# Kernel optimization log

Hardware: AMD Instinct MI355X
Metric: run time of the kernel (lower is better)

Reference implementation:

```python
import jax, jax.numpy as jnp
import numpy as np

HEADS = 4
KD = 32          # key_dim per head
LEVELS = 2
G = 3            # 2**dims - 1 HP orientation groups
STRENGTH = 0.25
DECAY = 0.6
LN_EPS = 1e-5
MIX_EPS = 1e-3


def _layernorm(x, g, b):
    m = jnp.mean(x, axis=-1, keepdims=True)
    v = jnp.var(x, axis=-1, keepdims=True)
    return (x - m) * jax.lax.rsqrt(v + LN_EPS) * g + b


def _dwt2(x):
    # Haar analysis, periodic/even sizes. [B,H,W,C] -> [B,H/2,W/2,4C] (LL,LH,HL,HH)
    x00 = x[:, 0::2, 0::2]; x01 = x[:, 0::2, 1::2]
    x10 = x[:, 1::2, 0::2]; x11 = x[:, 1::2, 1::2]
    ll = (x00 + x01 + x10 + x11) * 0.5
    lh = (x00 - x01 + x10 - x11) * 0.5
    hl = (x00 + x01 - x10 - x11) * 0.5
    hh = (x00 - x01 - x10 + x11) * 0.5
    return jnp.concatenate([ll, lh, hl, hh], axis=-1)


def _idwt2(w):
    # exact Haar synthesis: [B,H/2,W/2,4C] -> [B,H,W,C]
    ll, lh, hl, hh = jnp.split(w, 4, axis=-1)
    x00 = (ll + lh + hl + hh) * 0.5
    x01 = (ll - lh + hl - hh) * 0.5
    x10 = (ll + lh - hl - hh) * 0.5
    x11 = (ll - lh - hl + hh) * 0.5
    B, H2, W2, C = ll.shape
    r0 = jnp.stack([x00, x01], axis=3).reshape(B, H2, 2 * W2, C)  # interleave W
    r1 = jnp.stack([x10, x11], axis=3).reshape(B, H2, 2 * W2, C)
    return jnp.stack([r0, r1], axis=2).reshape(B, 2 * H2, 2 * W2, C)  # interleave H


def _axial_mhsa(x, p):
    # AxialMHSAND: sequential sweep over spatial axes; each pass is
    # proj(attn(softmax(QK^T/sqrt(d)) V)) on norm(x), qkv via 1x1 conv (=matmul).
    g, b, wq, bq, wk, bk, wv, bv, wp, bp = p
    scale = KD ** -0.5
    for axis in (1, 2):
        X = _layernorm(x, g, b)
        B, H, W, _ = X.shape
        Q = (X @ wq + bq).reshape(B, H, W, HEADS, KD)
        K = (X @ wk + bk).reshape(B, H, W, HEADS, KD)
        V = (X @ wv + bv).reshape(B, H, W, HEADS, KD)
        if axis == 1:  # attend along H, batch over (B, W, heads)
            A = jax.nn.softmax(jnp.einsum('bqwnd,bkwnd->bwnqk', Q, K) * scale, axis=-1)
            Y = jnp.einsum('bwnqk,bkwnd->bqwnd', A, V)
        else:          # attend along W, batch over (B, H, heads)
            A = jax.nn.softmax(jnp.einsum('bhqnd,bhknd->bhnqk', Q, K) * scale, axis=-1)
            Y = jnp.einsum('bhnqk,bhknd->bhqnd', A, V)
        x = Y.reshape(B, H, W, HEADS * KD) @ wp + bp
    return x


def setup_inputs() -> dict:
    key = jax.random.key(0)
    ks = jax.random.split(key, 24)
    C = 64
    HD = HEADS * KD
    s = 0.02
    inp = {'x': jax.random.normal(ks[0], (4, 256, 256, C), jnp.float32)}
    i = 1
    for pre in ('lp', 'hp'):
        inp[pre + '_ln_g'] = jnp.ones((C,), jnp.float32)
        inp[pre + '_ln_b'] = jnp.zeros((C,), jnp.float32)
        inp[pre + '_wq'] = jax.random.normal(ks[i], (C, HD), jnp.float32) * s
        inp[pre + '_bq'] = jax.random.normal(ks[i + 1], (HD,), jnp.float32) * s
        inp[pre + '_wk'] = jax.random.normal(ks[i + 2], (C, HD), jnp.float32) * s
        inp[pre + '_bk'] = jax.random.normal(ks[i + 3], (HD,), jnp.float32) * s
        inp[pre + '_wv'] = jax.random.normal(ks[i + 4], (C, HD), jnp.float32) * s
        inp[pre + '_bv'] = jax.random.normal(ks[i + 5], (HD,), jnp.float32) * s
        inp[pre + '_wp'] = jax.random.normal(ks[i + 6], (HD, C), jnp.float32) * s
        inp[pre + '_bp'] = jax.random.normal(ks[i + 7], (C,), jnp.float32) * s
        i += 8
    mix = jnp.eye(G, dtype=jnp.float32) + MIX_EPS * (jnp.ones((G, G), jnp.float32) - jnp.eye(G, dtype=jnp.float32))
    inp['mix_w0'] = mix
    inp['mix_w1'] = mix
    return inp


def reference(x, lp_ln_g, lp_ln_b, lp_wq, lp_bq, lp_wk, lp_bk, lp_wv, lp_bv, lp_wp, lp_bp,
              hp_ln_g, hp_ln_b, hp_wq, hp_bq, hp_wk, hp_bk, hp_wv, hp_bv, hp_wp, hp_bp,
              mix_w0, mix_w1):
    lp_p = (lp_ln_g, lp_ln_b, lp_wq, lp_bq, lp_wk, lp_bk, lp_wv, lp_bv, lp_wp, lp_bp)
    hp_p = (hp_ln_g, hp_ln_b, hp_wq, hp_bq, hp_wk, hp_bk, hp_wv, hp_bv, hp_wp, hp_bp)
    mix_ws = [mix_w0, mix_w1]
    C = x.shape[-1]
    cur = x
    hps = []
    for _ in range(LEVELS):  # analysis pyramid
        w = _dwt2(cur)
        hps.append(w[..., C:])
        cur = w[..., :C]
    # deepest LP: axial attention, residual with full strength
    cur = cur + STRENGTH * _axial_mhsa(cur, lp_p)
    for l in reversed(range(LEVELS)):  # synthesis with per-level HP processing
        hp = hps[l]
        B, H2, W2, _ = hp.shape
        gain = STRENGTH * (DECAY ** (LEVELS - 1 - l))  # coarser levels stronger
        hp_g = hp.reshape(B, H2, W2, G, C)
        mixed = jnp.einsum('gd,bhwdc->bhwgc', mix_ws[l], hp_g)  # OrientationMix
        batched = mixed.transpose(3, 0, 1, 2, 4).reshape(G * B, H2, W2, C)
        att = _axial_mhsa(batched, hp_p)  # shared hp_attn across groups/levels
        att = att.reshape(G, B, H2, W2, C).transpose(1, 2, 3, 0, 4).reshape(B, H2, W2, G * C)
        hp_out = hp + gain * att
        cur = _idwt2(jnp.concatenate([cur, hp_out], axis=-1))
    return cur
```

## Files before the change

### kernel.cpp

```cpp
#include <hip/hip_runtime.h>

#define LN_EPS 1e-5f

typedef __attribute__((ext_vector_type(8))) short bf16x8;
typedef __attribute__((ext_vector_type(4))) float f32x4;

#define MFMA16(A, B, C) __builtin_amdgcn_mfma_f32_16x16x32_bf16(A, B, C, 0, 0, 0)

static __device__ __forceinline__ unsigned short f2bf_rne(float f) {
    union { unsigned int i; float f; } c; c.f = f;
    unsigned int i = c.i;
    return (unsigned short)((i + 0x7fffu + ((i >> 16) & 1u)) >> 16);
}
static __device__ __forceinline__ void bfstore2(unsigned short* p, float x, float y) {
    *(unsigned int*)p = (unsigned int)f2bf_rne(x) | ((unsigned int)f2bf_rne(y) << 16);
}
static __device__ __forceinline__ unsigned pk2(float a, float b) {
    return __builtin_amdgcn_perm(__builtin_bit_cast(unsigned, b),
                                 __builtin_bit_cast(unsigned, a), 0x07060302u);
}
static __device__ __forceinline__ unsigned short tb16(float f) {
    return (unsigned short)(__builtin_bit_cast(unsigned, f) >> 16);
}

__global__ void dwt_kernel(const float4* __restrict__ in, float4* __restrict__ ll,
                           float4* __restrict__ hp, int B, int H2, int W2) {
    const int i = blockIdx.x * blockDim.x + threadIdx.x;
    const int total = B * H2 * W2 * 16;
    if (i >= total) return;
    const int c4 = i & 15;
    int t = i >> 4;
    const int w2 = t % W2; t /= W2;
    const int h2 = t % H2;
    const int b = t / H2;
    const int W = W2 * 2;
    const size_t base = (((size_t)b * (H2 * 2) + 2 * h2) * W + 2 * w2) * 16 + c4;
    const float4 x00 = in[base];
    const float4 x01 = in[base + 16];
    const float4 x10 = in[base + (size_t)W * 16];
    const float4 x11 = in[base + (size_t)W * 16 + 16];
    float4 vll, vlh, vhl, vhh;
#define DWTC(a) \
    vll.a = (x00.a + x01.a + x10.a + x11.a) * 0.5f; \
    vlh.a = (x00.a - x01.a + x10.a - x11.a) * 0.5f; \
    vhl.a = (x00.a + x01.a - x10.a - x11.a) * 0.5f; \
    vhh.a = (x00.a - x01.a - x10.a + x11.a) * 0.5f;
    DWTC(x) DWTC(y) DWTC(z) DWTC(w)
#undef DWTC
    const size_t oi = ((size_t)b * H2 + h2) * W2 + w2;
    ll[oi * 16 + c4] = vll;
    hp[oi * 48 + c4] = vlh;
    hp[oi * 48 + 16 + c4] = vhl;
    hp[oi * 48 + 32 + c4] = vhh;
}

__global__ void idwt_kernel(const float4* __restrict__ cur, const float4* __restrict__ hp,
                            const float4* __restrict__ att, float gain,
                            float4* __restrict__ out, int B, int H2, int W2) {
    const int i = blockIdx.x * blockDim.x + threadIdx.x;
    const int total = B * H2 * W2 * 16;
    if (i >= total) return;
    const int c4 = i & 15;
    int t = i >> 4;
    const int w2 = t % W2; t /= W2;
    const int h2 = t % H2;
    const int b = t / H2;
    const size_t oi = ((size_t)b * H2 + h2) * W2 + w2;
    const size_t sp = (size_t)h2 * W2 + w2;
    const size_t gstr = (size_t)B * H2 * W2;
    const float4 vll = cur[oi * 16 + c4];
    float4 vlh = hp[oi * 48 + c4];
    float4 vhl = hp[oi * 48 + 16 + c4];
    float4 vhh = hp[oi * 48 + 32 + c4];
    const float4 a0 = att[((size_t)b * H2 * W2 + sp) * 16 + c4];
    const float4 a1 = att[((size_t)b * H2 * W2 + gstr + sp) * 16 + c4];
    const float4 a2 = att[((size_t)b * H2 * W2 + 2 * gstr + sp) * 16 + c4];
#define ADDG(a) \
    vlh.a = fmaf(gain, a0.a, vlh.a); \
    vhl.a = fmaf(gain, a1.a, vhl.a); \
    vhh.a = fmaf(gain, a2.a, vhh.a);
    ADDG(x) ADDG(y) ADDG(z) ADDG(w)
#undef ADDG
    float4 x00, x01, x10, x11;
#define IDWTC(a) \
    x00.a = (vll.a + vlh.a + vhl.a + vhh.a) * 0.5f; \
    x01.a = (vll.a - vlh.a + vhl.a - vhh.a) * 0.5f; \
    x10.a = (vll.a + vlh.a - vhl.a - vhh.a) * 0.5f; \
    x11.a = (vll.a - vlh.a - vhl.a + vhh.a) * 0.5f;
    IDWTC(x) IDWTC(y) IDWTC(z) IDWTC(w)
#undef IDWTC
    const int W = W2 * 2;
    const size_t r0 = (((size_t)b * (H2 * 2) + 2 * h2) * W + 2 * w2) * 16 + c4;
    out[r0] = x00;
    out[r0 + 16] = x01;
    out[r0 + (size_t)W * 16] = x10;
    out[r0 + (size_t)W * 16 + 16] = x11;
}

__global__ void mix_kernel(const float4* __restrict__ hp, const float* __restrict__ mixw,
                           float4* __restrict__ outb, int B, int HW) {
    const int i = blockIdx.x * blockDim.x + threadIdx.x;
    const int total = 3 * B * HW * 16;
    if (i >= total) return;
    const int c4 = i & 15;
    int t = i >> 4;
    const int p = t % HW; t /= HW;
    const int b = t % B;
    const int g = t / B;
    const float m0 = mixw[g * 3 + 0];
    const float m1 = mixw[g * 3 + 1];
    const float m2 = mixw[g * 3 + 2];
    const size_t hb = ((size_t)b * HW + p) * 48 + c4;
    const float4 h0 = hp[hb];
    const float4 h1 = hp[hb + 16];
    const float4 h2 = hp[hb + 32];
    float4 r;
    r.x = m0 * h0.x + m1 * h1.x + m2 * h2.x;
    r.y = m0 * h0.y + m1 * h1.y + m2 * h2.y;
    r.z = m0 * h0.z + m1 * h1.z + m2 * h2.z;
    r.w = m0 * h0.w + m1 * h1.w + m2 * h2.w;
    outb[i] = r;
}

__global__ void prep_weights(const float* __restrict__ lwq, const float* __restrict__ lwk,
                             const float* __restrict__ lwv, const float* __restrict__ lwp,
                             const float* __restrict__ hwq, const float* __restrict__ hwk,
                             const float* __restrict__ hwv, const float* __restrict__ hwp,
                             unsigned short* __restrict__ wbuf) {
    const int i = blockIdx.x * blockDim.x + threadIdx.x;
    if (i >= 65536) return;
    const int set = i >> 15;
    const int r = i & 32767;
    const float* wq = set ? hwq : lwq;
    const float* wk = set ? hwk : lwk;
    const float* wv = set ? hwv : lwv;
    const float* wp = set ? hwp : lwp;
    float v;
    if (r < 24576) {
        const int nn = r >> 6, c = r & 63;
        const float* w = (nn < 128) ? wq : (nn < 256) ? wk : wv;
        v = w[c * 128 + (nn & 127)];
    } else {
        const int r2 = r - 24576;
        const int nn = r2 >> 7, d = r2 & 127;
        v = wp[d * 64 + nn];
    }
    wbuf[i] = f2bf_rne(v);
}

template<int S>
__global__ __launch_bounds__(S * 4)
void axial_attn(const float* __restrict__ xin, float* __restrict__ xout,
                const float* __restrict__ basep, float res_scale, int axis,
                const float* __restrict__ ln_g, const float* __restrict__ ln_b,
                const float* __restrict__ bq, const float* __restrict__ bk,
                const float* __restrict__ bv, const float* __restrict__ bp,
                const unsigned short* __restrict__ wqkvT,
                const unsigned short* __restrict__ wpT)
{
    constexpr int BS = S * 4;
    constexpr int NW = BS / 64;
    constexpr int XSTR = 72;
    constexpr int QSTR = 136;
    constexpr int PSTR = S + 8;
    constexpr int NTPW = 24 / NW;

    __shared__ __align__(16) unsigned short Xs[S * XSTR];
    __shared__ __align__(16) unsigned short Qs[S * QSTR];
    __shared__ __align__(16) unsigned short Ks[S * QSTR];
    __shared__ __align__(16) unsigned short Vt[128 * PSTR];
    __shared__ __align__(16) unsigned short Pb[NW * 16 * PSTR];

    const int tid = threadIdx.x;
    const int lane = tid & 63;
    const int w = tid >> 6;
    const int n16 = lane & 15;
    const int quad = lane >> 4;

    const int line = blockIdx.x;
    const int lb = line / S;
    const int lr = line - lb * S;
    size_t lbase, tstr;
    if (axis == 1) { lbase = ((size_t)lb * S * S + lr) * 64; tstr = (size_t)S * 64; }
    else           { lbase = ((size_t)lb * S + lr) * (size_t)S * 64; tstr = 64; }

    {
        const float4* x4 = (const float4*)xin;
        const size_t lbase4 = lbase >> 2, tstr4 = tstr >> 2;
        const int sub = tid & 15;
        const float4 g4 = ((const float4*)ln_g)[sub];
        const float4 be4 = ((const float4*)ln_b)[sub];
        for (int t = (tid >> 4); t < S; t += BS / 16) {
            float4 v = x4[lbase4 + (size_t)t * tstr4 + sub];
            float s = v.x + v.y + v.z + v.w;
            float ss = v.x * v.x + v.y * v.y + v.z * v.z + v.w * v.w;
            #pragma unroll
            for (int m = 1; m < 16; m <<= 1) {
                s += __shfl_xor(s, m);
                ss += __shfl_xor(ss, m);
            }
            const float mean = s * 0.015625f;
            const float rstd = rsqrtf(ss * 0.015625f - mean * mean + LN_EPS);
            unsigned short* xr = &Xs[t * XSTR + sub * 4];
            bfstore2(xr,     (v.x - mean) * rstd * g4.x + be4.x,
                             (v.y - mean) * rstd * g4.y + be4.y);
            bfstore2(xr + 2, (v.z - mean) * rstd * g4.z + be4.z,
                             (v.w - mean) * rstd * g4.w + be4.w);
        }
    }
    __syncthreads();

    {
        for (int i = 0; i < NTPW; ++i) {
            const int nt = w * NTPW + i;
            const int region = nt >> 3;
            const int cbase = (nt & 7) * 16;
            const float* bias_base = (region == 0) ? bq : (region == 1) ? bk : bv;
            const float bias = bias_base[cbase + n16];
            const bf16x8 B0 = *(const bf16x8*)&wqkvT[(nt * 16 + n16) * 64 + quad * 8];
            const bf16x8 B1 = *(const bf16x8*)&wqkvT[(nt * 16 + n16) * 64 + 32 + quad * 8];
            for (int mt = 0; mt < S / 16; ++mt) {
                const bf16x8 A0 = *(const bf16x8*)&Xs[(mt * 16 + n16) * XSTR + quad * 8];
                const bf16x8 A1 = *(const bf16x8*)&Xs[(mt * 16 + n16) * XSTR + 32 + quad * 8];
                f32x4 acc = {bias, bias, bias, bias};
                acc = MFMA16(A0, B0, acc);
                acc = MFMA16(A1, B1, acc);
                if (region < 2) {
                    unsigned short* dst = (region == 0) ? Qs : Ks;
                    const int row0 = mt * 16 + quad * 4;
                    #pragma unroll
                    for (int r = 0; r < 4; ++r)
                        dst[(row0 + r) * QSTR + cbase + n16] = tb16(acc[r]);
                } else {
                    const int d = cbase + n16;
                    const unsigned p01 = pk2(acc[0], acc[1]);
                    const unsigned p23 = pk2(acc[2], acc[3]);
                    *(uint2*)&Vt[d * PSTR + mt * 16 + quad * 4] = make_uint2(p01, p23);
                }
            }
        }
    }
    __syncthreads();

    {
        constexpr int WPH = NW / 4;
        const int h = w / WPH;
        const int sub = w - h * WPH;
        const int hoff = h * 32;
        unsigned short* pbw = &Pb[w * 16 * PSTR];
        const float qs = 0.17677669529663687f * 1.4426950408889634f;
        const bf16x8 ones = (bf16x8)(short)0x3F80;

        bf16x8 vb[2][S / 32];
        #pragma unroll
        for (int nt2 = 0; nt2 < 2; ++nt2)
            #pragma unroll
            for (int kt = 0; kt < S / 32; ++kt)
                vb[nt2][kt] = *(const bf16x8*)&Vt[(hoff + nt2 * 16 + n16) * PSTR + kt * 32 + quad * 8];

        for (int si = 0; si < 4; ++si) {
            const int q0 = (sub * 4 + si) * 16;
            const bf16x8 qb = *(const bf16x8*)&Qs[(q0 + n16) * QSTR + hoff + quad * 8];
            for (int mt = 0; mt < S / 16; ++mt) {
                const bf16x8 ka = *(const bf16x8*)&Ks[(mt * 16 + n16) * QSTR + hoff + quad * 8];
                f32x4 sc = {0.f, 0.f, 0.f, 0.f};
                sc = MFMA16(ka, qb, sc);
                const float e0 = __builtin_amdgcn_exp2f(sc[0] * qs);
                const float e1 = __builtin_amdgcn_exp2f(sc[1] * qs);
                const float e2 = __builtin_amdgcn_exp2f(sc[2] * qs);
                const float e3 = __builtin_amdgcn_exp2f(sc[3] * qs);
                *(uint2*)&pbw[n16 * PSTR + mt * 16 + quad * 4] =
                    make_uint2(pk2(e0, e1), pk2(e2, e3));
            }
            f32x4 accl = {0.f, 0.f, 0.f, 0.f};
            f32x4 y0 = {0.f, 0.f, 0.f, 0.f};
            f32x4 y1 = {0.f, 0.f, 0.f, 0.f};
            for (int kt = 0; kt < S / 32; ++kt) {
                const bf16x8 pa = *(const bf16x8*)&pbw[n16 * PSTR + kt * 32 + quad * 8];
                accl = MFMA16(pa, ones, accl);
                y0 = MFMA16(pa, vb[0][kt], y0);
                y1 = MFMA16(pa, vb[1][kt], y1);
            }
            #pragma unroll
            for (int r = 0; r < 4; ++r) {
                const float inv = __builtin_amdgcn_rcpf(accl[r]);
                const int row = q0 + quad * 4 + r;
                Qs[row * QSTR + hoff + n16]      = tb16(y0[r] * inv);
                Qs[row * QSTR + hoff + 16 + n16] = tb16(y1[r] * inv);
            }
        }
    }
    __syncthreads();

    {
        const int m0 = w * 16;
        bf16x8 pa[4];
        #pragma unroll
        for (int kt = 0; kt < 4; ++kt)
            pa[kt] = *(const bf16x8*)&Qs[(m0 + n16) * QSTR + kt * 32 + quad * 8];
        #pragma unroll
        for (int nt = 0; nt < 4; ++nt) {
            const float bias = bp[nt * 16 + n16];
            f32x4 acc = {bias, bias, bias, bias};
            #pragma unroll
            for (int kt = 0; kt < 4; ++kt) {
                const bf16x8 wb = *(const bf16x8*)&wpT[(nt * 16 + n16) * 128 + kt * 32 + quad * 8];
                acc = MFMA16(pa[kt], wb, acc);
            }
            #pragma unroll
            for (int r = 0; r < 4; ++r) {
                const size_t gi = lbase + (size_t)(m0 + quad * 4 + r) * tstr + nt * 16 + n16;
                float v = acc[r];
                if (basep) v = fmaf(res_scale, v, basep[gi]);
                xout[gi] = v;
            }
        }
    }
}

extern "C" void kernel_launch(void* const* d_in, const int* in_sizes, int n_in,
                              void* d_out, int out_size, void* d_ws, size_t ws_size,
                              hipStream_t stream) {
    (void)in_sizes; (void)n_in; (void)out_size; (void)ws_size;
    const float* x = (const float*)d_in[0];
    const float* P_lp[10];
    const float* P_hp[10];
    for (int i = 0; i < 10; ++i) P_lp[i] = (const float*)d_in[1 + i];
    for (int i = 0; i < 10; ++i) P_hp[i] = (const float*)d_in[11 + i];
    const float* mw0 = (const float*)d_in[21];
    const float* mw1 = (const float*)d_in[22];
    float* out = (float*)d_out;
    float* ws = (float*)d_ws;

    float* ll0 = ws;
    float* hp0 = ll0 + (size_t)4194304;
    float* t0  = hp0 + (size_t)12582912;
    float* ll1  = t0;
    float* hp1  = t0 + (size_t)1048576;
    float* ta2  = t0 + (size_t)4194304;
    float* lpta = t0 + (size_t)7340032;
    float* tb  = out;
    float* t1b = out;
    unsigned short* wbuf = (unsigned short*)(out + (size_t)13631488);

    prep_weights<<<256, 256, 0, stream>>>(
        P_lp[2], P_lp[4], P_lp[6], P_lp[8],
        P_hp[2], P_hp[4], P_hp[6], P_hp[8], wbuf);

    dwt_kernel<<<4 * 128 * 128 * 16 / 256, 256, 0, stream>>>(
        (const float4*)x, (float4*)ll0, (float4*)hp0, 4, 128, 128);
    dwt_kernel<<<4 * 64 * 64 * 16 / 256, 256, 0, stream>>>(
        (const float4*)ll0, (float4*)ll1, (float4*)hp1, 4, 64, 64);

    const unsigned short* lp_qkvT = wbuf;
    const unsigned short* lp_wpT  = wbuf + 24576;
    const unsigned short* hp_qkvT = wbuf + 32768;
    const unsigned short* hp_wpT  = wbuf + 32768 + 24576;

#define ATTN(S_, GRID_, XIN_, XOUT_, BASE_, RS_, P_, QKVT_, WPT_, AX_) \
    axial_attn<S_><<<GRID_, (S_) * 4, 0, stream>>>(XIN_, XOUT_, BASE_, RS_, AX_, \
        P_[0], P_[1], P_[3], P_[5], P_[7], P_[9], QKVT_, WPT_)

    ATTN(64, 4 * 64, ll1, lpta, (const float*)nullptr, 1.f, P_lp, lp_qkvT, lp_wpT, 1);
    ATTN(64, 4 * 64, lpta, ll1, ll1, 0.25f, P_lp, lp_qkvT, lp_wpT, 2);

    mix_kernel<<<3 * 4 * 64 * 64 * 16 / 256, 256, 0, stream>>>(
        (const float4*)hp1, mw1, (float4*)ta2, 4, 64 * 64);
    ATTN(64, 12 * 64, ta2, tb, (const float*)nullptr, 1.f, P_hp, hp_qkvT, hp_wpT, 1);
    ATTN(64, 12 * 64, tb, ta2, (const float*)nullptr, 1.f, P_hp, hp_qkvT, hp_wpT, 2);
    idwt_kernel<<<4 * 64 * 64 * 16 / 256, 256, 0, stream>>>(
        (const float4*)ll1, (const float4*)hp1, (const float4*)ta2, 0.25f,
        (float4*)ll0, 4, 64, 64);

    mix_kernel<<<3 * 4 * 128 * 128 * 16 / 256, 256, 0, stream>>>(
        (const float4*)hp0, mw0, (float4*)t0, 4, 128 * 128);
    ATTN(128, 12 * 128, t0, t1b, (const float*)nullptr, 1.f, P_hp, hp_qkvT, hp_wpT, 1);
    ATTN(128, 12 * 128, t1b, t0, (const float*)nullptr, 1.f, P_hp, hp_qkvT, hp_wpT, 2);
    idwt_kernel<<<4 * 128 * 128 * 16 / 256, 256, 0, stream>>>(
        (const float4*)ll0, (const float4*)hp0, (const float4*)t0, 0.15f,
        (float4*)out, 4, 128, 128);
#undef ATTN
}
```

Measured before the change: 486.7 us.

## Fuse orientation mix into attention, batch LP/HP passes, fold softmax scale into Wq

Removes the standalone mix kernels by computing the orientation mix inside the attention load stage. The LP and level-1 HP attention passes now run as one grouped launch using a job struct, which cuts launches and fills the GPU better. The softmax scale times log2(e) is folded into the Q weights and bias, removing a multiply before exp2. The QKV projection loop is restructured so B fragments stay in registers, K fragments are hoisted into registers, and launch bounds request 2 blocks per CU, which raises register pressure.

```diff
diff --git a/kernel.cpp b/kernel.cpp
--- a/kernel.cpp
+++ b/kernel.cpp
@@ -1,6 +1,7 @@
 #include <hip/hip_runtime.h>
 
 #define LN_EPS 1e-5f
+#define QSCALE 0.25500526578425445f
 
 typedef __attribute__((ext_vector_type(8))) short bf16x8;
 typedef __attribute__((ext_vector_type(4))) float f32x4;
@@ -97,31 +98,6 @@
     out[r0 + (size_t)W * 16 + 16] = x11;
 }
 
-__global__ void mix_kernel(const float4* __restrict__ hp, const float* __restrict__ mixw,
-                           float4* __restrict__ outb, int B, int HW) {
-    const int i = blockIdx.x * blockDim.x + threadIdx.x;
-    const int total = 3 * B * HW * 16;
-    if (i >= total) return;
-    const int c4 = i & 15;
-    int t = i >> 4;
-    const int p = t % HW; t /= HW;
-    const int b = t % B;
-    const int g = t / B;
-    const float m0 = mixw[g * 3 + 0];
-    const float m1 = mixw[g * 3 + 1];
-    const float m2 = mixw[g * 3 + 2];
-    const size_t hb = ((size_t)b * HW + p) * 48 + c4;
-    const float4 h0 = hp[hb];
-    const float4 h1 = hp[hb + 16];
-    const float4 h2 = hp[hb + 32];
-    float4 r;
-    r.x = m0 * h0.x + m1 * h1.x + m2 * h2.x;
-    r.y = m0 * h0.y + m1 * h1.y + m2 * h2.y;
-    r.z = m0 * h0.z + m1 * h1.z + m2 * h2.z;
-    r.w = m0 * h0.w + m1 * h1.w + m2 * h2.w;
-    outb[i] = r;
-}
-
 __global__ void prep_weights(const float* __restrict__ lwq, const float* __restrict__ lwk,
                              const float* __restrict__ lwv, const float* __restrict__ lwp,
                              const float* __restrict__ hwq, const float* __restrict__ hwk,
@@ -140,6 +116,7 @@
         const int nn = r >> 6, c = r & 63;
         const float* w = (nn < 128) ? wq : (nn < 256) ? wk : wv;
         v = w[c * 128 + (nn & 127)];
+        if (nn < 128) v *= QSCALE;
     } else {
         const int r2 = r - 24576;
         const int nn = r2 >> 7, d = r2 & 127;
@@ -148,15 +125,22 @@
     wbuf[i] = f2bf_rne(v);
 }
 
+struct Job {
+    const float* xin;
+    const float* mixsrc;
+    const float* mixw;
+    float* xout;
+    const float* basep;
+    float res_scale;
+    const float* ln_g; const float* ln_b;
+    const float* bq; const float* bk; const float* bv; const float* bp;
+    const unsigned short* wqkvT;
+    const unsigned short* wpT;
+};
+
 template<int S>
-__global__ __launch_bounds__(S * 4)
-void axial_attn(const float* __restrict__ xin, float* __restrict__ xout,
-                const float* __restrict__ basep, float res_scale, int axis,
-                const float* __restrict__ ln_g, const float* __restrict__ ln_b,
-                const float* __restrict__ bq, const float* __restrict__ bk,
-                const float* __restrict__ bv, const float* __restrict__ bp,
-                const unsigned short* __restrict__ wqkvT,
-                const unsigned short* __restrict__ wpT)
+__global__ __launch_bounds__(S * 4, 2)
+void axial_attn(Job jA, Job jB, int nA, int axis)
 {
     constexpr int BS = S * 4;
     constexpr int NW = BS / 64;
@@ -177,7 +161,9 @@
     const int n16 = lane & 15;
     const int quad = lane >> 4;
 
-    const int line = blockIdx.x;
+    const bool isB = (int)blockIdx.x >= nA;
+    const Job j = isB ? jB : jA;
+    const int line = isB ? (int)blockIdx.x - nA : (int)blockIdx.x;
     const int lb = line / S;
     const int lr = line - lb * S;
     size_t lbase, tstr;
@@ -185,13 +171,33 @@
     else           { lbase = ((size_t)lb * S + lr) * (size_t)S * 64; tstr = 64; }
 
     {
-        const float4* x4 = (const float4*)xin;
+        const int sub = tid & 15;
+        const float4 g4 = ((const float4*)j.ln_g)[sub];
+        const float4 be4 = ((const float4*)j.ln_b)[sub];
+        const float4* x4 = (const float4*)j.xin;
+        const float4* hp4 = (const float4*)j.mixsrc;
         const size_t lbase4 = lbase >> 2, tstr4 = tstr >> 2;
-        const int sub = tid & 15;
-        const float4 g4 = ((const float4*)ln_g)[sub];
-        const float4 be4 = ((const float4*)ln_b)[sub];
+        float m0, m1, m2; int bimg;
+        if (hp4) {
+            const int g = lb >> 2;
+            bimg = lb & 3;
+            m0 = j.mixw[g * 3 + 0]; m1 = j.mixw[g * 3 + 1]; m2 = j.mixw[g * 3 + 2];
+        }
         for (int t = (tid >> 4); t < S; t += BS / 16) {
-            float4 v = x4[lbase4 + (size_t)t * tstr4 + sub];
+            float4 v;
+            if (hp4) {
+                const int pos = (axis == 1) ? (t * S + lr) : (lr * S + t);
+                const size_t hb = ((size_t)bimg * S * S + pos) * 48 + sub;
+                const float4 h0 = hp4[hb];
+                const float4 h1 = hp4[hb + 16];
+                const float4 h2 = hp4[hb + 32];
+                v.x = m0 * h0.x + m1 * h1.x + m2 * h2.x;
+                v.y = m0 * h0.y + m1 * h1.y + m2 * h2.y;
+                v.z = m0 * h0.z + m1 * h1.z + m2 * h2.z;
+                v.w = m0 * h0.w + m1 * h1.w + m2 * h2.w;
+            } else {
+                v = x4[lbase4 + (size_t)t * tstr4 + sub];
+            }
             float s = v.x + v.y + v.z + v.w;
             float ss = v.x * v.x + v.y * v.y + v.z * v.z + v.w * v.w;
             #pragma unroll
@@ -211,20 +217,31 @@
     __syncthreads();
 
     {
+        bf16x8 Bf0[NTPW], Bf1[NTPW];
+        float biasv[NTPW];
+        #pragma unroll
         for (int i = 0; i < NTPW; ++i) {
             const int nt = w * NTPW + i;
             const int region = nt >> 3;
             const int cbase = (nt & 7) * 16;
-            const float* bias_base = (region == 0) ? bq : (region == 1) ? bk : bv;
-            const float bias = bias_base[cbase + n16];
-            const bf16x8 B0 = *(const bf16x8*)&wqkvT[(nt * 16 + n16) * 64 + quad * 8];
-            const bf16x8 B1 = *(const bf16x8*)&wqkvT[(nt * 16 + n16) * 64 + 32 + quad * 8];
-            for (int mt = 0; mt < S / 16; ++mt) {
-                const bf16x8 A0 = *(const bf16x8*)&Xs[(mt * 16 + n16) * XSTR + quad * 8];
-                const bf16x8 A1 = *(const bf16x8*)&Xs[(mt * 16 + n16) * XSTR + 32 + quad * 8];
-                f32x4 acc = {bias, bias, bias, bias};
-                acc = MFMA16(A0, B0, acc);
-                acc = MFMA16(A1, B1, acc);
+            const float* bias_base = (region == 0) ? j.bq : (region == 1) ? j.bk : j.bv;
+            float bias = bias_base[cbase + n16];
+            if (region == 0) bias *= QSCALE;
+            biasv[i] = bias;
+            Bf0[i] = *(const bf16x8*)&j.wqkvT[(nt * 16 + n16) * 64 + quad * 8];
+            Bf1[i] = *(const bf16x8*)&j.wqkvT[(nt * 16 + n16) * 64 + 32 + quad * 8];
+        }
+        for (int mt = 0; mt < S / 16; ++mt) {
+            const bf16x8 A0 = *(const bf16x8*)&Xs[(mt * 16 + n16) * XSTR + quad * 8];
+            const bf16x8 A1 = *(const bf16x8*)&Xs[(mt * 16 + n16) * XSTR + 32 + quad * 8];
+            #pragma unroll
+            for (int i = 0; i < NTPW; ++i) {
+                const int nt = w * NTPW + i;
+                const int region = nt >> 3;
+                const int cbase = (nt & 7) * 16;
+                f32x4 acc = {biasv[i], biasv[i], biasv[i], biasv[i]};
+                acc = MFMA16(A0, Bf0[i], acc);
+                acc = MFMA16(A1, Bf1[i], acc);
                 if (region < 2) {
                     unsigned short* dst = (region == 0) ? Qs : Ks;
                     const int row0 = mt * 16 + quad * 4;
@@ -233,9 +250,8 @@
                         dst[(row0 + r) * QSTR + cbase + n16] = tb16(acc[r]);
                 } else {
                     const int d = cbase + n16;
-                    const unsigned p01 = pk2(acc[0], acc[1]);
-                    const unsigned p23 = pk2(acc[2], acc[3]);
-                    *(uint2*)&Vt[d * PSTR + mt * 16 + quad * 4] = make_uint2(p01, p23);
+                    *(uint2*)&Vt[d * PSTR + mt * 16 + quad * 4] =
+                        make_uint2(pk2(acc[0], acc[1]), pk2(acc[2], acc[3]));
                 }
             }
         }
@@ -248,38 +264,43 @@
         const int sub = w - h * WPH;
         const int hoff = h * 32;
         unsigned short* pbw = &Pb[w * 16 * PSTR];
-        const float qs = 0.17677669529663687f * 1.4426950408889634f;
         const bf16x8 ones = (bf16x8)(short)0x3F80;
 
-        bf16x8 vb[2][S / 32];
-        #pragma unroll
-        for (int nt2 = 0; nt2 < 2; ++nt2)
-            #pragma unroll
-            for (int kt = 0; kt < S / 32; ++kt)
-                vb[nt2][kt] = *(const bf16x8*)&Vt[(hoff + nt2 * 16 + n16) * PSTR + kt * 32 + quad * 8];
-
+        bf16x8 vb0[S / 32], vb1[S / 32];
+        #pragma unroll
+        for (int kt = 0; kt < S / 32; ++kt) {
+            vb0[kt] = *(const bf16x8*)&Vt[(hoff + n16) * PSTR + kt * 32 + quad * 8];
+            vb1[kt] = *(const bf16x8*)&Vt[(hoff + 16 + n16) * PSTR + kt * 32 + quad * 8];
+        }
+        bf16x8 ka[S / 16];
+        #pragma unroll
+        for (int mt = 0; mt < S / 16; ++mt)
+            ka[mt] = *(const bf16x8*)&Ks[(mt * 16 + n16) * QSTR + hoff + quad * 8];
+
+        #pragma unroll
         for (int si = 0; si < 4; ++si) {
             const int q0 = (sub * 4 + si) * 16;
             const bf16x8 qb = *(const bf16x8*)&Qs[(q0 + n16) * QSTR + hoff + quad * 8];
+            #pragma unroll
             for (int mt = 0; mt < S / 16; ++mt) {
-                const bf16x8 ka = *(const bf16x8*)&Ks[(mt * 16 + n16) * QSTR + hoff + quad * 8];
                 f32x4 sc = {0.f, 0.f, 0.f, 0.f};
-                sc = MFMA16(ka, qb, sc);
-                const float e0 = __builtin_amdgcn_exp2f(sc[0] * qs);
-                const float e1 = __builtin_amdgcn_exp2f(sc[1] * qs);
-                const float e2 = __builtin_amdgcn_exp2f(sc[2] * qs);
-                const float e3 = __builtin_amdgcn_exp2f(sc[3] * qs);
+                sc = MFMA16(ka[mt], qb, sc);
+                const float e0 = __builtin_amdgcn_exp2f(sc[0]);
+                const float e1 = __builtin_amdgcn_exp2f(sc[1]);
+                const float e2 = __builtin_amdgcn_exp2f(sc[2]);
+                const float e3 = __builtin_amdgcn_exp2f(sc[3]);
                 *(uint2*)&pbw[n16 * PSTR + mt * 16 + quad * 4] =
                     make_uint2(pk2(e0, e1), pk2(e2, e3));
             }
             f32x4 accl = {0.f, 0.f, 0.f, 0.f};
             f32x4 y0 = {0.f, 0.f, 0.f, 0.f};
             f32x4 y1 = {0.f, 0.f, 0.f, 0.f};
+            #pragma unroll
             for (int kt = 0; kt < S / 32; ++kt) {
                 const bf16x8 pa = *(const bf16x8*)&pbw[n16 * PSTR + kt * 32 + quad * 8];
                 accl = MFMA16(pa, ones, accl);
-                y0 = MFMA16(pa, vb[0][kt], y0);
-                y1 = MFMA16(pa, vb[1][kt], y1);
+                y0 = MFMA16(pa, vb0[kt], y0);
+                y1 = MFMA16(pa, vb1[kt], y1);
             }
             #pragma unroll
             for (int r = 0; r < 4; ++r) {
@@ -300,19 +321,19 @@
             pa[kt] = *(const bf16x8*)&Qs[(m0 + n16) * QSTR + kt * 32 + quad * 8];
         #pragma unroll
         for (int nt = 0; nt < 4; ++nt) {
-            const float bias = bp[nt * 16 + n16];
+            const float bias = j.bp[nt * 16 + n16];
             f32x4 acc = {bias, bias, bias, bias};
             #pragma unroll
             for (int kt = 0; kt < 4; ++kt) {
-                const bf16x8 wb = *(const bf16x8*)&wpT[(nt * 16 + n16) * 128 + kt * 32 + quad * 8];
+                const bf16x8 wb = *(const bf16x8*)&j.wpT[(nt * 16 + n16) * 128 + kt * 32 + quad * 8];
                 acc = MFMA16(pa[kt], wb, acc);
             }
             #pragma unroll
             for (int r = 0; r < 4; ++r) {
                 const size_t gi = lbase + (size_t)(m0 + quad * 4 + r) * tstr + nt * 16 + n16;
                 float v = acc[r];
-                if (basep) v = fmaf(res_scale, v, basep[gi]);
-                xout[gi] = v;
+                if (j.basep) v = fmaf(j.res_scale, v, j.basep[gi]);
+                j.xout[gi] = v;
             }
         }
     }
@@ -357,27 +378,38 @@
     const unsigned short* hp_qkvT = wbuf + 32768;
     const unsigned short* hp_wpT  = wbuf + 32768 + 24576;
 
-#define ATTN(S_, GRID_, XIN_, XOUT_, BASE_, RS_, P_, QKVT_, WPT_, AX_) \
-    axial_attn<S_><<<GRID_, (S_) * 4, 0, stream>>>(XIN_, XOUT_, BASE_, RS_, AX_, \
-        P_[0], P_[1], P_[3], P_[5], P_[7], P_[9], QKVT_, WPT_)
-
-    ATTN(64, 4 * 64, ll1, lpta, (const float*)nullptr, 1.f, P_lp, lp_qkvT, lp_wpT, 1);
-    ATTN(64, 4 * 64, lpta, ll1, ll1, 0.25f, P_lp, lp_qkvT, lp_wpT, 2);
-
-    mix_kernel<<<3 * 4 * 64 * 64 * 16 / 256, 256, 0, stream>>>(
-        (const float4*)hp1, mw1, (float4*)ta2, 4, 64 * 64);
-    ATTN(64, 12 * 64, ta2, tb, (const float*)nullptr, 1.f, P_hp, hp_qkvT, hp_wpT, 1);
-    ATTN(64, 12 * 64, tb, ta2, (const float*)nullptr, 1.f, P_hp, hp_qkvT, hp_wpT, 2);
+    auto mkjob = [](const float* xin, const float* mixsrc, const float* mixw,
+                    float* xout, const float* basep, float rs,
+                    const float* const* P, const unsigned short* qkvT,
+                    const unsigned short* wpT) {
+        Job jj;
+        jj.xin = xin; jj.mixsrc = mixsrc; jj.mixw = mixw;
+        jj.xout = xout; jj.basep = basep; jj.res_scale = rs;
+        jj.ln_g = P[0]; jj.ln_b = P[1];
+        jj.bq = P[3]; jj.bk = P[5]; jj.bv = P[7]; jj.bp = P[9];
+        jj.wqkvT = qkvT; jj.wpT = wpT;
+        return jj;
+    };
+
+    {
+        Job a1 = mkjob(ll1, nullptr, nullptr, lpta, nullptr, 1.f, P_lp, lp_qkvT, lp_wpT);
+        Job b1 = mkjob(nullptr, hp1, mw1, tb, nullptr, 1.f, P_hp, hp_qkvT, hp_wpT);
+        axial_attn<64><<<1024, 256, 0, stream>>>(a1, b1, 256, 1);
+        Job a2 = mkjob(lpta, nullptr, nullptr, ll1, ll1, 0.25f, P_lp, lp_qkvT, lp_wpT);
+        Job b2 = mkjob(tb, nullptr, nullptr, ta2, nullptr, 1.f, P_hp, hp_qkvT, hp_wpT);
+        axial_attn<64><<<1024, 256, 0, stream>>>(a2, b2, 256, 2);
+    }
     idwt_kernel<<<4 * 64 * 64 * 16 / 256, 256, 0, stream>>>(
         (const float4*)ll1, (const float4*)hp1, (const float4*)ta2, 0.25f,
         (float4*)ll0, 4, 64, 64);
 
-    mix_kernel<<<3 * 4 * 128 * 128 * 16 / 256, 256, 0, stream>>>(
-        (const float4*)hp0, mw0, (float4*)t0, 4, 128 * 128);
-    ATTN(128, 12 * 128, t0, t1b, (const float*)nullptr, 1.f, P_hp, hp_qkvT, hp_wpT, 1);
-    ATTN(128, 12 * 128, t1b, t0, (const float*)nullptr, 1.f, P_hp, hp_qkvT, hp_wpT, 2);
+    {
+        Job c1 = mkjob(nullptr, hp0, mw0, t1b, nullptr, 1.f, P_hp, hp_qkvT, hp_wpT);
+        axial_attn<128><<<1536, 512, 0, stream>>>(c1, c1, 1536, 1);
+        Job c2 = mkjob(t1b, nullptr, nullptr, t0, nullptr, 1.f, P_hp, hp_qkvT, hp_wpT);
+        axial_attn<128><<<1536, 512, 0, stream>>>(c2, c2, 1536, 2);
+    }
     idwt_kernel<<<4 * 128 * 128 * 16 / 256, 256, 0, stream>>>(
         (const float4*)ll0, (const float4*)hp0, (const float4*)t0, 0.15f,
         (float4*)out, 4, 128, 128);
-#undef ATTN
-}
+}
```

New measurement: 433.7 us. 1.12x faster.
